# Performance work log

Measured on AMD Instinct MI355X. Metric: run time of the kernel, lower is better.

## Reference

```python
import jax, jax.numpy as jnp
import numpy as np

STRIDE = 16
SIZES = np.array([128.0, 256.0, 512.0], np.float32)
RATIOS = np.array([0.5, 1.0, 2.0], np.float32)
N_POS, N_NEG = 32, 32          # n_sample=64, pos_ratio=0.5
POS_THR, NEG_THR = 0.7, 0.2
W_CONF, W_REG = 1.0, 5.0


def _conv(x, w, b, stride, pad):
    y = jax.lax.conv_general_dilated(x, w, (stride, stride), [(pad, pad), (pad, pad)],
                                     dimension_numbers=('NCHW', 'OIHW', 'NCHW'))
    return y + b[None, :, None, None]


def _anchors(fw, fh, stride):
    # 9 anchors per center: 3 sizes x 3 aspect ratios
    ws = (SIZES[:, None] * np.sqrt(RATIOS)[None, :]).reshape(-1)
    hs = (SIZES[:, None] / np.sqrt(RATIOS)[None, :]).reshape(-1)
    wh = jnp.asarray(np.stack([ws, hs], -1))                      # (9,2)
    cx = (jnp.arange(fw, dtype=jnp.float32) + 0.5) * stride
    cy = (jnp.arange(fh, dtype=jnp.float32) + 0.5) * stride
    gx, gy = jnp.meshgrid(cx, cy, indexing='ij')                  # x-major, like the torch list comp
    ctr = jnp.stack([gx, gy], -1)[:, :, None, :]                  # (fw,fh,1,2)
    tl = ctr - wh / 2.0
    xywh = jnp.concatenate([tl, jnp.broadcast_to(wh, tl.shape)], -1)  # (fw,fh,9,4)
    return xywh.reshape(-1, 4)


def _xywh_to_xyxy(b):
    return jnp.concatenate([b[:, :2], b[:, :2] + b[:, 2:]], -1)


def _iou(a, b):  # a [N,4], b [M,4], xyxy
    lt = jnp.maximum(a[:, None, :2], b[None, :, :2])
    rb = jnp.minimum(a[:, None, 2:], b[None, :, 2:])
    inter = jnp.clip(rb - lt, 0.0).prod(-1)
    aa = (a[:, 2] - a[:, 0]) * (a[:, 3] - a[:, 1])
    ab = (b[:, 2] - b[:, 0]) * (b[:, 3] - b[:, 1])
    return inter / (aa[:, None] + ab[None, :] - inter)


def _head_flat(y, per):  # [1, 9*per, H, W] -> [W*H*9, per], matching anchor flatten order
    _, _, H, W = y.shape
    return y[0].reshape(9, per, H, W).transpose(3, 2, 0, 1).reshape(-1, per)


def _apply_offsets(boxes, off):  # decode proposals from xyxy boxes + (dx,dy,dw,dh)
    w = boxes[:, 2] - boxes[:, 0]; h = boxes[:, 3] - boxes[:, 1]
    cx = boxes[:, 0] + 0.5 * w;    cy = boxes[:, 1] + 0.5 * h
    ncx = cx + off[:, 0] * w;      ncy = cy + off[:, 1] * h
    nw = w * jnp.exp(off[:, 2]);   nh = h * jnp.exp(off[:, 3])
    return jnp.stack([ncx - nw / 2, ncy - nh / 2, ncx + nw / 2, ncy + nh / 2], -1)


def _box_offset(anc, gt):
    aw = anc[:, 2] - anc[:, 0]; ah = anc[:, 3] - anc[:, 1]
    acx = anc[:, 0] + 0.5 * aw; acy = anc[:, 1] + 0.5 * ah
    gw = gt[:, 2] - gt[:, 0];   gh = gt[:, 3] - gt[:, 1]
    gcx = gt[:, 0] + 0.5 * gw;  gcy = gt[:, 1] + 0.5 * gh
    return jnp.stack([(gcx - acx) / aw, (gcy - acy) / ah,
                      jnp.log(gw / aw), jnp.log(gh / ah)], -1)


def setup_inputs():
    key = jax.random.key(0)
    ks = jax.random.split(key, 12)
    img_data = jax.random.normal(ks[0], (1, 3, 1600, 1600), jnp.float32)
    x1 = jax.random.uniform(ks[1], (64,), minval=0.0, maxval=1400.0)
    y1 = jax.random.uniform(ks[2], (64,), minval=0.0, maxval=1400.0)
    bw = jax.random.uniform(ks[3], (64,), minval=32.0, maxval=200.0)
    bh = jax.random.uniform(ks[4], (64,), minval=32.0, maxval=200.0)
    gt_boxes = jnp.stack([x1, y1, x1 + bw, y1 + bh], -1)[None]   # [1,64,4], all valid (no -1 pad)
    gt_classes = jax.random.randint(ks[5], (1, 64), 1, 21, jnp.int32)
    def w(k, shape, fan):
        return jax.random.normal(k, shape, jnp.float32) * np.float32(np.sqrt(2.0 / fan))
    return dict(
        img_data=img_data, gt_boxes=gt_boxes, gt_classes=gt_classes,
        w1=w(ks[6], (64, 3, 7, 7), 3 * 49),      b1=jnp.zeros(64, jnp.float32),
        w2=w(ks[7], (256, 64, 3, 3), 64 * 9),    b2=jnp.zeros(256, jnp.float32),
        w_rpn=w(ks[8], (256, 256, 3, 3), 256 * 9), b_rpn=jnp.zeros(256, jnp.float32),
        w_cls=w(ks[9], (18, 256, 1, 1), 256),    b_cls=jnp.zeros(18, jnp.float32),
        w_reg=w(ks[10], (36, 256, 1, 1), 256),   b_reg=jnp.zeros(36, jnp.float32),
    )


def reference(img_data, gt_boxes, gt_classes, w1, b1, w2, b2, w_rpn, b_rpn, w_cls, b_cls, w_reg, b_reg):
    # --- feature extractor (total stride 16) ---
    fm = jax.nn.relu(_conv(img_data, w1, b1, 4, 3))
    fm = jax.nn.relu(_conv(fm, w2, b2, 4, 1))            # [1,256,100,100]
    H, W = fm.shape[2], fm.shape[3]
    # --- anchors + IoU matching ---
    anchors_xywh = _anchors(W, H, STRIDE)                # [N,4] xywh
    anchors_xyxy = _xywh_to_xyxy(anchors_xywh)
    gt = gt_boxes[0]                                     # [M,4], all valid
    ious = _iou(anchors_xyxy, gt)                        # [N,M]
    N = ious.shape[0]
    gt_max = ious.max(0)                                 # best iou per gt
    is_gt_best = (ious == gt_max[None, :]).any(1)        # torch: where(iou == gt_max)[0]
    anc_argmax = ious.argmax(1)
    anc_max = ious.max(1)
    labels = jnp.full((N,), -1.0, jnp.float32)
    labels = jnp.where(anc_max < NEG_THR, 0.0, labels)
    labels = jnp.where(is_gt_best, 1.0, labels)
    labels = jnp.where(anc_max > POS_THR, 1.0, labels)
    # --- deterministic pos/neg sampling (fixed sizes; replaces randperm subsampling) ---
    idx = jnp.arange(N, dtype=jnp.float32)
    _, pos_index = jax.lax.top_k(jnp.where(labels == 1.0, anc_max, -1.0), N_POS)
    _, neg_index = jax.lax.top_k(jnp.where(labels == 0.0, 1e6 - idx, -1e9), N_NEG)
    bboxes_pos = anchors_xyxy[pos_index]                 # box_convert(xywh->xyxy) of pos anchors
    # --- proposal module (RPN head) ---
    h = jax.nn.relu(_conv(fm, w_rpn, b_rpn, 1, 1))
    cls = _head_flat(_conv(h, w_cls, b_cls, 1, 0), 2)    # [N,2]
    reg = _head_flat(_conv(h, w_reg, b_reg, 1, 0), 4)    # [N,4]
    pos_score = cls[pos_index]
    neg_score = cls[neg_index]
    offset_pos = reg[pos_index]
    proposals = _apply_offsets(bboxes_pos, offset_pos)
    # --- losses ---
    gt_offset = _box_offset(bboxes_pos, gt[anc_argmax[pos_index]])
    logits = jnp.concatenate([pos_score, neg_score], 0)  # [64,2]
    tgt = jnp.concatenate([jnp.ones(N_POS, jnp.int32), jnp.zeros(N_NEG, jnp.int32)])
    logp = jax.nn.log_softmax(logits, -1)
    cls_loss = -logp[jnp.arange(N_POS + N_NEG), tgt].mean()
    d = gt_offset - offset_pos
    ad = jnp.abs(d)
    reg_loss = jnp.where(ad < 1.0, 0.5 * d * d, ad - 0.5).mean()
    total_rpn_loss = W_CONF * cls_loss + W_REG * reg_loss
    gt_cls_pos = gt_classes[0][anc_argmax[pos_index]]
    return (total_rpn_loss, fm, proposals, pos_index, gt_cls_pos)
```

## Files before the change

kernel.cpp:

```cpp
#include <hip/hip_runtime.h>
#include <math.h>


#define CAP 4096

typedef __attribute__((ext_vector_type(8))) short bf16x8;
typedef __attribute__((ext_vector_type(4))) float f32x4;

#define OFF_F1T     0
#define OFF_HBUF    0
#define OFF_FMT     5171328
#define OFF_CPART   6503040
#define OFF_RPART   7223040
#define OFF_WA1     8663040
#define OFF_W9_2    8672448
#define OFF_W9_3    8746176
#define OFF_WTC     9041088
#define OFF_WTG     9045696
#define OFF_AARG    9054912
#define OFF_NEGM    9144912
#define OFF_POSM    9147728
#define OFF_GTMAX   9150544
#define OFF_CANDS   9150688
#define OFF_CANDI   9154784

__device__ __forceinline__ unsigned short f2bf(float f) {
    unsigned int u = __float_as_uint(f);
    u += 0x7fffu + ((u >> 16) & 1u);
    return (unsigned short)(u >> 16);
}

__device__ __forceinline__ void anchor_box(int i, float& x0, float& y0,
                                           float& x1, float& y1, float& area) {
#pragma clang fp contract(off)
    const float sizes[3]  = {128.f, 256.f, 512.f};
    const float ratios[3] = {0.5f, 1.f, 2.f};
    int a = i % 9;
    int q = i / 9;
    int iy = q % 100;
    int ix = q / 100;
    int s = a / 3, r = a % 3;
    float sq = sqrtf(ratios[r]);
    float w = sizes[s] * sq;
    float h = sizes[s] / sq;
    float cx = ((float)ix + 0.5f) * 16.0f;
    float cy = ((float)iy + 0.5f) * 16.0f;
    x0 = cx - w * 0.5f;
    y0 = cy - h * 0.5f;
    x1 = x0 + w;
    y1 = y0 + h;
    area = (x1 - x0) * (y1 - y0);
}

__device__ __forceinline__ float iou_one(float ax0, float ay0, float ax1, float ay1, float aa,
                                         float bx0, float by0, float bx1, float by1, float ab) {
#pragma clang fp contract(off)
    float ltx = fmaxf(ax0, bx0), lty = fmaxf(ay0, by0);
    float rbx = fminf(ax1, bx1), rby = fminf(ay1, by1);
    float iw = fmaxf(rbx - ltx, 0.0f);
    float ih = fmaxf(rby - lty, 0.0f);
    float inter = iw * ih;
    return inter / ((aa + ab) - inter);
}

__global__ __launch_bounds__(256) void setup_kernel(const float* __restrict__ wc, float* __restrict__ wtc,
                                                    const float* __restrict__ wg, float* __restrict__ wtg,
                                                    const float* __restrict__ w1, unsigned short* __restrict__ wa1,
                                                    const float* __restrict__ w2, unsigned short* __restrict__ w9_2,
                                                    const float* __restrict__ wr, unsigned short* __restrict__ w9_3,
                                                    unsigned int* __restrict__ f1t_u, unsigned int* __restrict__ fmt_u,
                                                    unsigned int* __restrict__ gtmax) {
    int i = blockIdx.x * 256 + threadIdx.x;
    if (i < 65) { gtmax[i] = 0u; return; }
    i -= 65;
    if (i < 103040) {
        if (i < 51328) {
            int p = i >> 5, part = i & 31;
            int x, y;
            if (p < 804) { y = (p < 402) ? 0 : 401; x = p % 402; }
            else { int j = p - 804; x = (j < 400) ? 0 : 401; y = 1 + (j % 400); }
            f1t_u[(y * 402 + x) * 32 + part] = 0u;
        } else {
            int i2 = i - 51328;
            int p = i2 >> 7, part = i2 & 127;
            int x, y;
            if (p < 204) { y = (p < 102) ? 0 : 101; x = p % 102; }
            else { int j = p - 204; x = (j < 100) ? 0 : 101; y = 1 + (j % 100); }
            fmt_u[(y * 102 + x) * 128 + part] = 0u;
        }
        return;
    }
    i -= 103040;
    if (i < 4608) { int c = i / 256, k = i - c * 256; wtc[k * 18 + c] = wc[i]; return; }
    i -= 4608;
    if (i < 9216) { int c = i / 256, k = i - c * 256; wtg[k * 36 + c] = wg[i]; return; }
    i -= 9216;
    if (i < 12288) {
        int oc = i / 192, k = i - oc * 192;
        int q = k >> 3, kx = k & 7;
        int ky = q / 3, ic = q - (q / 3) * 3;
        wa1[i] = (q < 21 && kx < 7) ? f2bf(w1[oc * 147 + ic * 49 + ky * 7 + kx])
                                    : (unsigned short)0;
        return;
    }
    i -= 12288;
    if (i < 147456) {
        int cc = i >> 14;
        int rem = i & 16383;
        int ocT = rem >> 10;
        int rem2 = rem & 1023;
        int kcl = rem2 >> 9;
        int lane = (rem2 & 511) >> 3;
        int e = rem2 & 7;
        int oc = ocT * 16 + (lane & 15);
        int ic = kcl * 32 + (lane >> 4) * 8 + e;
        w9_2[i] = f2bf(w2[(oc * 64 + ic) * 9 + cc]);
        return;
    }
    i -= 147456;
    if (i < 589824) {
        int cc = i >> 14;
        int rem = i & 16383;
        int ocT = rem >> 10;
        int rem2 = rem & 1023;
        int kcl = rem2 >> 9;
        int lane = (rem2 & 511) >> 3;
        int e = rem2 & 7;
        int kk = cc >> 2, chv = cc & 3;
        int oc = ocT * 16 + (lane & 15);
        int icl = kcl * 32 + (lane >> 4) * 8 + e;
        w9_3[i] = f2bf(wr[(oc * 256 + chv * 64 + icl) * 9 + kk]);
    }
}

__global__ __launch_bounds__(256) void conv1_mfma(const float* __restrict__ img,
                                                  const unsigned short* __restrict__ wA,
                                                  const float* __restrict__ bias,
                                                  unsigned short* __restrict__ f1t) {
    __shared__ unsigned short win[24 * 260];
    __shared__ unsigned short tileT[64 * 72];
    int t = threadIdx.x;
    int wave = t >> 6, lane = t & 63;
    int quad = lane >> 4, l16 = lane & 15;
    int oy = blockIdx.y;
    int ox0 = blockIdx.x * 64;
    int gx0 = ox0 * 4 - 3;
    int gy0 = 4 * oy - 3;

    int gx = gx0 + t;
    bool xok = (gx >= 0) && (gx < 1600);
    float v[21];
#pragma unroll
    for (int r = 0; r < 21; r++) {
        int ky = r / 3, ic = r - (r / 3) * 3;
        int gy = gy0 + ky;
        v[r] = (xok && gy >= 0 && gy < 1600) ? img[(ic * 1600 + gy) * 1600 + gx] : 0.f;
    }
    float vt = 0.f;
    int rt = t >> 2, ctl = 256 + (t & 3);
    if (rt < 21) {
        int ky = rt / 3, ic = rt - (rt / 3) * 3;
        int gy = gy0 + ky;
        int gxt = gx0 + ctl;
        vt = (gxt >= 0 && gxt < 1600 && gy >= 0 && gy < 1600)
                 ? img[(ic * 1600 + gy) * 1600 + gxt] : 0.f;
    }
    bf16x8 afr[6];
    {
        const bf16x8* ap = (const bf16x8*)(wA + (wave * 16 + l16) * 192 + quad * 8);
#pragma unroll
        for (int c = 0; c < 6; c++) afr[c] = ap[c * 4];
    }
#pragma unroll
    for (int r = 0; r < 21; r++) win[r * 260 + t] = f2bf(v[r]);
    if (rt < 21) win[rt * 260 + ctl] = f2bf(vt);
    win[5460 + t] = 0;
    win[5460 + 256 + t] = 0;
    win[5460 + 512 + t] = 0;
    if (t < 12) win[5460 + 768 + t] = 0;
    __syncthreads();

    f32x4 acc[4];
#pragma unroll
    for (int j = 0; j < 4; j++) acc[j] = (f32x4){0.f, 0.f, 0.f, 0.f};
#pragma unroll
    for (int ch = 0; ch < 6; ch++) {
        const unsigned short* wrow = win + (ch * 4 + quad) * 260;
#pragma unroll
        for (int j = 0; j < 4; j++) {
            int px = j * 16 + l16;
            const unsigned long long* bp = (const unsigned long long*)(wrow + 4 * px);
            union { unsigned long long u[2]; bf16x8 v; } uu;
            uu.u[0] = bp[0];
            uu.u[1] = bp[1];
            acc[j] = __builtin_amdgcn_mfma_f32_16x16x32_bf16(afr[ch], uu.v, acc[j], 0, 0, 0);
        }
    }
#pragma unroll
    for (int reg = 0; reg < 4; reg++) {
        int oc = wave * 16 + quad * 4 + reg;
        float bv = bias[oc];
#pragma unroll
        for (int j = 0; j < 4; j++) {
            int px = j * 16 + l16;
            tileT[px * 72 + oc] = f2bf(fmaxf(acc[j][reg] + bv, 0.f));
        }
    }
    __syncthreads();
    int px = t >> 2, part = t & 3;
    int ox = ox0 + px;
    if (ox < 400) {
        int row = (oy + 1) * 402 + ox + 1;
        uint4 v0 = *(const uint4*)(tileT + px * 72 + part * 16);
        uint4 v1 = *(const uint4*)(tileT + px * 72 + part * 16 + 8);
        *(uint4*)(f1t + row * 64 + part * 16) = v0;
        *(uint4*)(f1t + row * 64 + part * 16 + 8) = v1;
    }
}

template<int ICC, int RS, int S, bool WRT>
__global__ __launch_bounds__(256, 3) void conv_gemm(const unsigned short* __restrict__ Bt,
                                                    const unsigned short* __restrict__ A9,
                                                    const float* __restrict__ bias,
                                                    float* __restrict__ outF,
                                                    unsigned short* __restrict__ outT) {
    const int NC = ICC / 64;
    const int HC = S * 24 + 3;
    const int LROW = ICC + 8;
    const int CHW = ICC / 8;
    const int TOT = 3 * HC * CHW;
    const int NIT = (TOT + 255) / 256;
    __shared__ unsigned short blds[3 * HC * LROW];
    int t = threadIdx.x;
    int xs = blockIdx.x, y = blockIdx.y;

    uint4 stg[NIT];
#pragma unroll
    for (int i = 0; i < NIT; i++) {
        int idx = t + i * 256;
        if (idx < TOT) {
            int row = idx / CHW, e = idx - row * CHW;
            int ky = row / HC, c = row - ky * HC;
            stg[i] = ((const uint4*)(Bt + ((size_t)(S * y + ky) * RS + S * xs * 25 + c) * ICC))[e];
        }
    }
#pragma unroll
    for (int i = 0; i < NIT; i++) {
        int idx = t + i * 256;
        if (idx < TOT) {
            int row = idx / CHW, e = idx - row * CHW;
            int ky = row / HC, c = row - ky * HC;
            int e2 = (S == 4) ? (e ^ ((c >> 2) & 7)) : e;
            *(uint4*)(blds + row * LROW + e2 * 8) = stg[i];
        }
    }

    int wave = t >> 6, lane = t & 63;
    int quad = lane >> 4, l16 = lane & 15;
    int oc0 = wave * 64;
    int pxe0 = min(l16, 24);
    int pxe1 = min(16 + l16, 24);
    int sw0 = pxe0 & 7, sw1 = pxe1 & 7;

    f32x4 acc[4][2];
#pragma unroll
    for (int mt = 0; mt < 4; mt++)
#pragma unroll
        for (int j = 0; j < 2; j++) acc[mt][j] = (f32x4){0.f, 0.f, 0.f, 0.f};

    const bf16x8* Av = (const bf16x8*)A9;
    int abase = wave * 512 + lane;
    __syncthreads();

    for (int cc = 0; cc < 9 * NC; cc++) {
        int pass = cc / NC, ch = cc - pass * NC;
        int ky = pass / 3, kx = pass - (pass / 3) * 3;
        bf16x8 af[4][2];
#pragma unroll
        for (int mt = 0; mt < 4; mt++)
#pragma unroll
            for (int kcl = 0; kcl < 2; kcl++)
                af[mt][kcl] = Av[abase + cc * 2048 + (mt * 2 + kcl) * 64];
        int rb0 = (ky * HC + S * pxe0 + kx) * LROW + ch * 64;
        int rb1 = (ky * HC + S * pxe1 + kx) * LROW + ch * 64;
#pragma unroll
        for (int kcl = 0; kcl < 2; kcl++) {
            int ck = kcl * 4 + quad;
            bf16x8 bf0 = *(const bf16x8*)(blds + rb0 + ((S == 4) ? (ck ^ sw0) : ck) * 8);
            bf16x8 bf1 = *(const bf16x8*)(blds + rb1 + ((S == 4) ? (ck ^ sw1) : ck) * 8);
#pragma unroll
            for (int mt = 0; mt < 4; mt++) {
                acc[mt][0] = __builtin_amdgcn_mfma_f32_16x16x32_bf16(af[mt][kcl], bf0, acc[mt][0], 0, 0, 0);
                acc[mt][1] = __builtin_amdgcn_mfma_f32_16x16x32_bf16(af[mt][kcl], bf1, acc[mt][1], 0, 0, 0);
            }
        }
    }
#pragma unroll
    for (int mt = 0; mt < 4; mt++) {
#pragma unroll
        for (int reg = 0; reg < 4; reg++) {
            int oc = oc0 + mt * 16 + quad * 4 + reg;
            float bv = bias[oc];
#pragma unroll
            for (int j = 0; j < 2; j++) {
                int pl = j * 16 + l16;
                if (pl < 25) {
                    int p = y * 100 + xs * 25 + pl;
                    float v = fmaxf(acc[mt][j][reg] + bv, 0.f);
                    outF[oc * 10000 + p] = v;
                    if (WRT) {
                        int r = (y + 1) * 102 + xs * 25 + pl + 1;
                        outT[r * 256 + oc] = f2bf(v);
                    }
                }
            }
        }
    }
}

__global__ __launch_bounds__(64) void head_kernel(const float* __restrict__ hbuf,
                                                  const float* __restrict__ wtc,
                                                  const float* __restrict__ wtg,
                                                  float* __restrict__ cpart,
                                                  float* __restrict__ rpart) {
    int p = blockIdx.x * 64 + threadIdx.x;
    int ch = blockIdx.y;
    int ic0 = ch * 64;
    if (p >= 10000) return;
    float acc[54];
#pragma unroll
    for (int j = 0; j < 54; j++) acc[j] = 0.f;
    for (int ic = 0; ic < 64; ic += 8) {
        float vv[8];
#pragma unroll
        for (int u = 0; u < 8; u++) vv[u] = hbuf[(ic0 + ic + u) * 10000 + p];
#pragma unroll
        for (int u = 0; u < 8; u++) {
            const float* wc_ = wtc + (ic0 + ic + u) * 18;
#pragma unroll
            for (int j = 0; j < 18; j++) acc[j] += vv[u] * wc_[j];
            const float* wg_ = wtg + (ic0 + ic + u) * 36;
#pragma unroll
            for (int j = 0; j < 36; j++) acc[18 + j] += vv[u] * wg_[j];
        }
    }
    for (int j = 0; j < 18; j++) cpart[(ch * 18 + j) * 10000 + p] = acc[j];
    for (int j = 0; j < 36; j++) rpart[(ch * 36 + j) * 10000 + p] = acc[18 + j];
}

__global__ __launch_bounds__(256) void iou_pass1(const float* __restrict__ gt,
                                                 int* __restrict__ aarg,
                                                 unsigned int* __restrict__ gtmax) {
    __shared__ float sg[64][4];
    __shared__ float sarea[64];
    __shared__ unsigned int smax[64];
    int t = threadIdx.x;
    if (t < 64) {
#pragma clang fp contract(off)
        float b0 = gt[t * 4 + 0], b1 = gt[t * 4 + 1];
        float b2 = gt[t * 4 + 2], b3 = gt[t * 4 + 3];
        sg[t][0] = b0; sg[t][1] = b1; sg[t][2] = b2; sg[t][3] = b3;
        sarea[t] = (b2 - b0) * (b3 - b1);
        smax[t] = 0u;
    }
    __syncthreads();
    int i = blockIdx.x * 256 + t;
    int iq = min(i, 89999);
    float x0, y0, x1, y1, aa;
    anchor_box(iq, x0, y0, x1, y1, aa);
    float best = -1.f;
    int bestj = 0;
    for (int j = 0; j < 64; j++) {
        float v = iou_one(x0, y0, x1, y1, aa, sg[j][0], sg[j][1], sg[j][2], sg[j][3], sarea[j]);
        if (v > best) { best = v; bestj = j; }
        float vm = v;
#pragma unroll
        for (int off = 32; off > 0; off >>= 1) vm = fmaxf(vm, __shfl_xor(vm, off));
        if ((t & 63) == 0) atomicMax(&smax[j], __float_as_uint(vm));
    }
    if (i < 90000) aarg[i] = bestj;
    __syncthreads();
    if (t < 64) atomicMax(&gtmax[t], smax[t]);
}

__global__ __launch_bounds__(256) void iou_pass2(const float* __restrict__ gt,
                                                 const unsigned int* __restrict__ gtmax,
                                                 unsigned long long* __restrict__ negmask,
                                                 unsigned long long* __restrict__ posmask,
                                                 float* __restrict__ cand_s,
                                                 int* __restrict__ cand_i,
                                                 unsigned int* __restrict__ cnt) {
    __shared__ float sg[64][4];
    __shared__ float sarea[64];
    __shared__ float sgm[64];
    int t = threadIdx.x;
    if (t < 64) {
#pragma clang fp contract(off)
        float b0 = gt[t * 4 + 0], b1 = gt[t * 4 + 1];
        float b2 = gt[t * 4 + 2], b3 = gt[t * 4 + 3];
        sg[t][0] = b0; sg[t][1] = b1; sg[t][2] = b2; sg[t][3] = b3;
        sarea[t] = (b2 - b0) * (b3 - b1);
        sgm[t] = __uint_as_float(gtmax[t]);
    }
    __syncthreads();
    int i = blockIdx.x * 256 + t;
    if (i >= 90000) return;
    float x0, y0, x1, y1, aa;
    anchor_box(i, x0, y0, x1, y1, aa);
    float best = -1.f;
    bool isbest = false;
    for (int j = 0; j < 64; j++) {
        float v = iou_one(x0, y0, x1, y1, aa, sg[j][0], sg[j][1], sg[j][2], sg[j][3], sarea[j]);
        if (v > best) best = v;
        if (v == sgm[j]) isbest = true;
    }
    float label = -1.f;
    if (best < 0.2f) label = 0.f;
    if (isbest) label = 1.f;
    if (best > 0.7f) label = 1.f;
    unsigned long long negb = __ballot(label == 0.f);
    unsigned long long posb = __ballot(label == 1.f);
    if ((t & 63) == 0) { negmask[i >> 6] = negb; posmask[i >> 6] = posb; }
    if (label == 1.f) {
        unsigned int p = atomicAdd(cnt, 1u);
        if (p < CAP) { cand_s[p] = best; cand_i[p] = i; }
    }
}

__device__ __forceinline__ unsigned long long shflx64(unsigned long long v, int m) {
    int lo = __shfl_xor((int)(unsigned)(v & 0xFFFFFFFFull), m);
    int hi = __shfl_xor((int)(unsigned)(v >> 32), m);
    return ((unsigned long long)(unsigned)hi << 32) | (unsigned)lo;
}

__device__ int wave_first32(const unsigned long long* __restrict__ mask,
                            bool invert, int* __restrict__ outIdx, int lane) {
    const int NW = 1407;
    const int WPT = 22;
    unsigned long long mw[WPT];
    int cnt = 0;
#pragma unroll
    for (int u = 0; u < WPT; u++) {
        int w = lane * WPT + u;
        unsigned long long m = 0ull;
        if (w < NW) {
            m = mask[w];
            if (invert) m = ~m;
            if (w == NW - 1) m &= 0xFFFFull;
        }
        mw[u] = m;
        cnt += __builtin_popcountll(m);
    }
    int inc = cnt;
#pragma unroll
    for (int off = 1; off < 64; off <<= 1) {
        int v = __shfl_up(inc, off);
        if (lane >= off) inc += v;
    }
    int total = __shfl(inc, 63);
    int pref = inc - cnt;
    if (pref < 32) {
#pragma unroll
        for (int u = 0; u < WPT; u++) {
            unsigned long long m = mw[u];
            int wbase = (lane * WPT + u) * 64;
            while (m && pref < 32) {
                int b = __builtin_ctzll(m);
                outIdx[pref++] = wbase + b;
                m &= m - 1;
            }
        }
    }
    return total;
}

__global__ __launch_bounds__(64) void tail_kernel(const unsigned long long* __restrict__ negmask,
                                                  const unsigned long long* __restrict__ posmask,
                                                  const float* __restrict__ cand_s,
                                                  const int* __restrict__ cand_i,
                                                  const unsigned int* __restrict__ cnt,
                                                  const float* __restrict__ cpart,
                                                  const float* __restrict__ rpart,
                                                  const float* __restrict__ bcls,
                                                  const float* __restrict__ breg,
                                                  const int* __restrict__ aarg,
                                                  const float* __restrict__ gt,
                                                  const int* __restrict__ gtc,
                                                  float* __restrict__ out) {
    __shared__ unsigned long long keys[CAP + 32];
    __shared__ int sfill[32];
    __shared__ int spidx[32];
    __shared__ int snidx[32];
    int lane = threadIdx.x;

    int ncand = min((int)*cnt, CAP);
    for (int c = lane; c < ncand; c += 64) {
        unsigned u = __float_as_uint(cand_s[c]);
        u ^= (u & 0x80000000u) ? 0xFFFFFFFFu : 0x80000000u;
        keys[c] = ((unsigned long long)u << 32) | (0xFFFFFFFFu - (unsigned)cand_i[c]);
    }
    int ntot = ncand;
    if (ncand < 32) {
        int tot = wave_first32(posmask, true, sfill, lane);
        int nfill = min(tot, 32);
        unsigned um1 = __float_as_uint(-1.0f) ^ 0xFFFFFFFFu;
        for (int k2 = lane; k2 < nfill; k2 += 64)
            keys[ncand + k2] = ((unsigned long long)um1 << 32) | (0xFFFFFFFFu - (unsigned)sfill[k2]);
        ntot += nfill;
    }

    unsigned long long lk = 0ull; int ls = -1;
    for (int c = lane; c < ntot; c += 64) {
        unsigned long long k = keys[c];
        if (k > lk) { lk = k; ls = c; }
    }
    for (int s = 0; s < 32; s++) {
        unsigned long long mk = lk;
#pragma unroll
        for (int off = 1; off < 64; off <<= 1) {
            unsigned long long o = shflx64(mk, off);
            if (o > mk) mk = o;
        }
        if (lk == mk && mk != 0ull) {
            spidx[s] = (int)(0xFFFFFFFFu - (unsigned)(mk & 0xFFFFFFFFull));
            keys[ls] = 0ull;
            lk = 0ull; ls = -1;
            for (int c = lane; c < ntot; c += 64) {
                unsigned long long k = keys[c];
                if (k > lk) { lk = k; ls = c; }
            }
        }
    }

    int totn = wave_first32(negmask, false, snidx, lane);
    if (lane == 0) {
        int nf = min(totn, 32);
        for (int s = nf; s < 32; s++) snidx[s] = s;
    }

    {
#pragma clang fp contract(off)
        const int PROP_OFF = 1 + 2560000;
        int t = lane;
        int n = (t < 32) ? spidx[t] : snidx[t - 32];
        int a = n % 9;
        int q = n / 9;
        int iy = q % 100;
        int ix = q / 100;
        int p = iy * 100 + ix;

        float l0 = bcls[a * 2 + 0], l1 = bcls[a * 2 + 1];
        for (int c = 0; c < 4; c++) {
            l0 += cpart[(c * 18 + a * 2 + 0) * 10000 + p];
            l1 += cpart[(c * 18 + a * 2 + 1) * 10000 + p];
        }
        float m = fmaxf(l0, l1);
        float lse = m + logf(expf(l0 - m) + expf(l1 - m));
        float logp = ((t < 32) ? l1 : l0) - lse;
        float cls_sum = logp;
#pragma unroll
        for (int off = 32; off > 0; off >>= 1) cls_sum += __shfl_down(cls_sum, off);

        float reg_sum = 0.f;
        if (t < 32) {
            float offv[4];
#pragma unroll
            for (int k = 0; k < 4; k++) {
                float v = breg[a * 4 + k];
                for (int c = 0; c < 4; c++) v += rpart[(c * 36 + a * 4 + k) * 10000 + p];
                offv[k] = v;
            }
            float x0, y0, x1, y1, aa;
            anchor_box(n, x0, y0, x1, y1, aa);
            float w = x1 - x0, h = y1 - y0;
            float cx = x0 + 0.5f * w, cy = y0 + 0.5f * h;
            float ncx = cx + offv[0] * w, ncy = cy + offv[1] * h;
            float nw = w * expf(offv[2]), nh = h * expf(offv[3]);
            out[PROP_OFF + t * 4 + 0] = ncx - nw * 0.5f;
            out[PROP_OFF + t * 4 + 1] = ncy - nh * 0.5f;
            out[PROP_OFF + t * 4 + 2] = ncx + nw * 0.5f;
            out[PROP_OFF + t * 4 + 3] = ncy + nh * 0.5f;

            int j = aarg[n];
            float g0 = gt[j * 4 + 0], g1 = gt[j * 4 + 1];
            float g2 = gt[j * 4 + 2], g3 = gt[j * 4 + 3];
            float gw = g2 - g0, gh = g3 - g1;
            float gcx = g0 + 0.5f * gw, gcy = g1 + 0.5f * gh;
            float tg[4];
            tg[0] = (gcx - cx) / w;
            tg[1] = (gcy - cy) / h;
            tg[2] = logf(gw / w);
            tg[3] = logf(gh / h);
#pragma unroll
            for (int k = 0; k < 4; k++) {
                float d = tg[k] - offv[k];
                float ad = fabsf(d);
                reg_sum += (ad < 1.f) ? 0.5f * d * d : ad - 0.5f;
            }
            out[PROP_OFF + 128 + t] = (float)n;
            out[PROP_OFF + 160 + t] = (float)gtc[j];
        }
#pragma unroll
        for (int off = 32; off > 0; off >>= 1) reg_sum += __shfl_down(reg_sum, off);
        if (t == 0) {
            float cls_loss = -(cls_sum / 64.f);
            float reg_loss = reg_sum / 128.f;
            out[0] = cls_loss + 5.f * reg_loss;
        }
    }
}

extern "C" void kernel_launch(void* const* d_in, const int* in_sizes, int n_in,
                              void* d_out, int out_size, void* d_ws, size_t ws_size,
                              hipStream_t stream) {
    const float* img = (const float*)d_in[0];
    const float* gt  = (const float*)d_in[1];
    const int*   gtc = (const int*)d_in[2];
    const float* w1  = (const float*)d_in[3];
    const float* b1  = (const float*)d_in[4];
    const float* w2  = (const float*)d_in[5];
    const float* b2  = (const float*)d_in[6];
    const float* wr  = (const float*)d_in[7];
    const float* br  = (const float*)d_in[8];
    const float* wc  = (const float*)d_in[9];
    const float* bc  = (const float*)d_in[10];
    const float* wg  = (const float*)d_in[11];
    const float* bg  = (const float*)d_in[12];
    float* out = (float*)d_out;
    float* ws = (float*)d_ws;

    unsigned short* f1t  = (unsigned short*)(ws + OFF_F1T);
    unsigned short* fmt  = (unsigned short*)(ws + OFF_FMT);
    unsigned short* wa1  = (unsigned short*)(ws + OFF_WA1);
    unsigned short* w9_2 = (unsigned short*)(ws + OFF_W9_2);
    unsigned short* w9_3 = (unsigned short*)(ws + OFF_W9_3);
    float* hbuf  = ws + OFF_HBUF;
    float* cpart = ws + OFF_CPART;
    float* rpart = ws + OFF_RPART;
    float* wtc   = ws + OFF_WTC;
    float* wtg   = ws + OFF_WTG;
    int*   aarg  = (int*)(ws + OFF_AARG);
    unsigned long long* negm = (unsigned long long*)(ws + OFF_NEGM);
    unsigned long long* posm = (unsigned long long*)(ws + OFF_POSM);
    unsigned int* gtmax = (unsigned int*)(ws + OFF_GTMAX);
    unsigned int* cnt   = gtmax + 64;
    float* cands = ws + OFF_CANDS;
    int*   candi = (int*)(ws + OFF_CANDI);
    float* fm    = out + 1;

    setup_kernel<<<dim3(3385), dim3(256), 0, stream>>>(wc, wtc, wg, wtg, w1, wa1,
                                                       w2, w9_2, wr, w9_3,
                                                       (unsigned int*)f1t, (unsigned int*)fmt, gtmax);

    conv1_mfma<<<dim3(7, 400), dim3(256), 0, stream>>>(img, wa1, b1, f1t);
    conv_gemm<64, 402, 4, true><<<dim3(4, 100), dim3(256), 0, stream>>>(f1t, w9_2, b2, fm, fmt);
    conv_gemm<256, 102, 1, false><<<dim3(4, 100), dim3(256), 0, stream>>>(fmt, w9_3, br, hbuf, nullptr);
    head_kernel<<<dim3(157, 4), dim3(64), 0, stream>>>(hbuf, wtc, wtg, cpart, rpart);

    iou_pass1<<<dim3(352), dim3(256), 0, stream>>>(gt, aarg, gtmax);
    iou_pass2<<<dim3(352), dim3(256), 0, stream>>>(gt, gtmax, negm, posm, cands, candi, cnt);
    tail_kernel<<<dim3(1), dim3(64), 0, stream>>>(negm, posm, cands, candi, cnt,
                                                  cpart, rpart, bc, bg, aarg, gt, gtc, out);
}
```

Before: 303.5 us.

## Split conv_gemm K reduction across two wave groups with LDS reduction

Doubles the conv_gemm block size to 512 threads. The 8 waves are split into two K-groups that each handle half of the reduction: half the channel chunks for the 256-channel conv, or one of the two k-slices for the 64-channel conv. Partial accumulators are then summed through shared memory before the bias/ReLU epilogue. The goal is more waves per block to hide latency on the 400-block launch, at the cost of an extra LDS reduction, two barriers and higher per-block register demand.

Result: faster. 280.6 us (-7.6%).

```diff
diff --git a/kernel.cpp b/kernel.cpp
--- a/kernel.cpp
+++ b/kernel.cpp
@@ -219,7 +219,7 @@
 }
 
 template<int ICC, int RS, int S, bool WRT>
-__global__ __launch_bounds__(256, 3) void conv_gemm(const unsigned short* __restrict__ Bt,
+__global__ __launch_bounds__(512, 4) void conv_gemm(const unsigned short* __restrict__ Bt,
                                                     const unsigned short* __restrict__ A9,
                                                     const float* __restrict__ bias,
                                                     float* __restrict__ outF,
@@ -229,15 +229,15 @@
     const int LROW = ICC + 8;
     const int CHW = ICC / 8;
     const int TOT = 3 * HC * CHW;
-    const int NIT = (TOT + 255) / 256;
-    __shared__ unsigned short blds[3 * HC * LROW];
+    const int NIT = (TOT + 511) / 512;
+    __shared__ __align__(16) unsigned short blds[3 * HC * LROW];
     int t = threadIdx.x;
     int xs = blockIdx.x, y = blockIdx.y;
 
     uint4 stg[NIT];
 #pragma unroll
     for (int i = 0; i < NIT; i++) {
-        int idx = t + i * 256;
+        int idx = t + i * 512;
         if (idx < TOT) {
             int row = idx / CHW, e = idx - row * CHW;
             int ky = row / HC, c = row - ky * HC;
@@ -246,18 +246,19 @@
     }
 #pragma unroll
     for (int i = 0; i < NIT; i++) {
-        int idx = t + i * 256;
+        int idx = t + i * 512;
         if (idx < TOT) {
             int row = idx / CHW, e = idx - row * CHW;
-            int ky = row / HC, c = row - ky * HC;
+            int c = row % HC;
             int e2 = (S == 4) ? (e ^ ((c >> 2) & 7)) : e;
             *(uint4*)(blds + row * LROW + e2 * 8) = stg[i];
         }
     }
 
     int wave = t >> 6, lane = t & 63;
+    int ow = wave & 3, kg = wave >> 2;
     int quad = lane >> 4, l16 = lane & 15;
-    int oc0 = wave * 64;
+    int oc0 = ow * 64;
     int pxe0 = min(l16, 24);
     int pxe1 = min(16 + l16, 24);
     int sw0 = pxe0 & 7, sw1 = pxe1 & 7;
@@ -269,48 +270,69 @@
         for (int j = 0; j < 2; j++) acc[mt][j] = (f32x4){0.f, 0.f, 0.f, 0.f};
 
     const bf16x8* Av = (const bf16x8*)A9;
-    int abase = wave * 512 + lane;
-    __syncthreads();
-
-    for (int cc = 0; cc < 9 * NC; cc++) {
+    __syncthreads();
+
+    const int CC0 = (NC == 1) ? 0 : kg * 18;
+    const int CC1 = (NC == 1) ? 9 : kg * 18 + 18;
+    const int KL0 = (NC == 1) ? kg : 0;
+    const int KL1 = (NC == 1) ? kg + 1 : 2;
+
+    for (int cc = CC0; cc < CC1; cc++) {
         int pass = cc / NC, ch = cc - pass * NC;
         int ky = pass / 3, kx = pass - (pass / 3) * 3;
-        bf16x8 af[4][2];
-#pragma unroll
-        for (int mt = 0; mt < 4; mt++)
-#pragma unroll
-            for (int kcl = 0; kcl < 2; kcl++)
-                af[mt][kcl] = Av[abase + cc * 2048 + (mt * 2 + kcl) * 64];
         int rb0 = (ky * HC + S * pxe0 + kx) * LROW + ch * 64;
         int rb1 = (ky * HC + S * pxe1 + kx) * LROW + ch * 64;
-#pragma unroll
-        for (int kcl = 0; kcl < 2; kcl++) {
+        for (int kcl = KL0; kcl < KL1; kcl++) {
+            bf16x8 af[4];
+#pragma unroll
+            for (int mt = 0; mt < 4; mt++)
+                af[mt] = Av[(size_t)cc * 2048 + (ow * 4 + mt) * 128 + kcl * 64 + lane];
             int ck = kcl * 4 + quad;
             bf16x8 bf0 = *(const bf16x8*)(blds + rb0 + ((S == 4) ? (ck ^ sw0) : ck) * 8);
             bf16x8 bf1 = *(const bf16x8*)(blds + rb1 + ((S == 4) ? (ck ^ sw1) : ck) * 8);
 #pragma unroll
             for (int mt = 0; mt < 4; mt++) {
-                acc[mt][0] = __builtin_amdgcn_mfma_f32_16x16x32_bf16(af[mt][kcl], bf0, acc[mt][0], 0, 0, 0);
-                acc[mt][1] = __builtin_amdgcn_mfma_f32_16x16x32_bf16(af[mt][kcl], bf1, acc[mt][1], 0, 0, 0);
+                acc[mt][0] = __builtin_amdgcn_mfma_f32_16x16x32_bf16(af[mt], bf0, acc[mt][0], 0, 0, 0);
+                acc[mt][1] = __builtin_amdgcn_mfma_f32_16x16x32_bf16(af[mt], bf1, acc[mt][1], 0, 0, 0);
             }
         }
     }
-#pragma unroll
-    for (int mt = 0; mt < 4; mt++) {
-#pragma unroll
-        for (int reg = 0; reg < 4; reg++) {
-            int oc = oc0 + mt * 16 + quad * 4 + reg;
-            float bv = bias[oc];
+
+    __syncthreads();
+    float* sred = (float*)blds;
+    if (kg == 1) {
+#pragma unroll
+        for (int mt = 0; mt < 4; mt++)
+#pragma unroll
+            for (int j = 0; j < 2; j++)
+                *(f32x4*)(sred + ((((ow * 4 + mt) * 2 + j) * 64 + lane) * 4)) = acc[mt][j];
+    }
+    __syncthreads();
+    if (kg == 0) {
+#pragma unroll
+        for (int mt = 0; mt < 4; mt++)
 #pragma unroll
             for (int j = 0; j < 2; j++) {
-                int pl = j * 16 + l16;
-                if (pl < 25) {
-                    int p = y * 100 + xs * 25 + pl;
-                    float v = fmaxf(acc[mt][j][reg] + bv, 0.f);
-                    outF[oc * 10000 + p] = v;
-                    if (WRT) {
-                        int r = (y + 1) * 102 + xs * 25 + pl + 1;
-                        outT[r * 256 + oc] = f2bf(v);
+                f32x4 o = *(const f32x4*)(sred + ((((ow * 4 + mt) * 2 + j) * 64 + lane) * 4));
+                acc[mt][j] = acc[mt][j] + o;
+            }
+#pragma unroll
+        for (int mt = 0; mt < 4; mt++) {
+#pragma unroll
+            for (int reg = 0; reg < 4; reg++) {
+                int oc = oc0 + mt * 16 + quad * 4 + reg;
+                float bv = bias[oc];
+#pragma unroll
+                for (int j = 0; j < 2; j++) {
+                    int pl = j * 16 + l16;
+                    if (pl < 25) {
+                        int p = y * 100 + xs * 25 + pl;
+                        float v = fmaxf(acc[mt][j][reg] + bv, 0.f);
+                        outF[oc * 10000 + p] = v;
+                        if (WRT) {
+                            int r = (y + 1) * 102 + xs * 25 + pl + 1;
+                            outT[r * 256 + oc] = f2bf(v);
+                        }
                     }
                 }
             }
@@ -653,8 +675,8 @@
                                                        (unsigned int*)f1t, (unsigned int*)fmt, gtmax);
 
     conv1_mfma<<<dim3(7, 400), dim3(256), 0, stream>>>(img, wa1, b1, f1t);
-    conv_gemm<64, 402, 4, true><<<dim3(4, 100), dim3(256), 0, stream>>>(f1t, w9_2, b2, fm, fmt);
-    conv_gemm<256, 102, 1, false><<<dim3(4, 100), dim3(256), 0, stream>>>(fmt, w9_3, br, hbuf, nullptr);
+    conv_gemm<64, 402, 4, true><<<dim3(4, 100), dim3(512), 0, stream>>>(f1t, w9_2, b2, fm, fmt);
+    conv_gemm<256, 102, 1, false><<<dim3(4, 100), dim3(512), 0, stream>>>(fmt, w9_3, br, hbuf, nullptr);
     head_kernel<<<dim3(157, 4), dim3(64), 0, stream>>>(hbuf, wtc, wtg, cpart, rpart);
 
     iou_pass1<<<dim3(352), dim3(256), 0, stream>>>(gt, aarg, gtmax);
```
